# Kernel tuning notes

Measured on AMD Instinct MI355X. Metric: run time of the kernel, lower is better.

## Reference

```python
import jax, jax.numpy as jnp
import numpy as np

N = 50000  # num nodes


def _spmm(edge_index, edge_w, x):
    # sparse [N,N] @ dense [N,d] via gather + segment-sum
    row, col = edge_index[0], edge_index[1]
    msgs = edge_w[:, None] * x[col]                      # [E, d]
    return jax.ops.segment_sum(msgs, row, num_segments=N)


def setup_inputs() -> dict:
    key = jax.random.key(0)
    k1, k2, k3, k4, k5 = jax.random.split(key, 5)
    E1, E2, d = 800000, 1600000, 128
    x = jax.random.normal(k1, (N, d), dtype=jnp.float32)
    edge_index1 = jax.random.randint(k2, (2, E1), 0, N, dtype=jnp.int64)
    edge_w1 = jax.random.uniform(k3, (E1,), dtype=jnp.float32)
    edge_index2 = jax.random.randint(k4, (2, E2), 0, N, dtype=jnp.int64)
    edge_w2 = jax.random.uniform(k5, (E2,), dtype=jnp.float32)
    return {"x": x, "edge_index1": edge_index1, "edge_w1": edge_w1,
            "edge_index2": edge_index2, "edge_w2": edge_w2}


def reference(x, edge_index1, edge_w1, edge_index2, edge_w2):
    x1 = _spmm(edge_index1, edge_w1, x)   # adj_t  @ x  -> [N, d]
    x2 = _spmm(edge_index2, edge_w2, x)   # adj_t2 @ x  -> [N, d]
    return jnp.concatenate([x1, x2], axis=1)  # [N, 2d]
```

## Files before the change

### kernel.cpp

```cpp
#include <hip/hip_runtime.h>


#define N_NODES 50000
#define D 128
#define OUT_STRIDE 256

#define BSHIFT 6
#define BROWS 64
#define NBUCK ((N_NODES + BROWS - 1) >> BSHIFT)
#define BBITS 10
#define CHUNK 4096
#define NTHR 512
#define NWAVE 8
#define WSEG (CHUNK / NWAVE)
#define SITERS (WSEG / 64)
#define ACAP 3072

typedef float vf2 __attribute__((ext_vector_type(2)));

static inline size_t align256(size_t x) { return (x + 255) & ~(size_t)255; }

__device__ __forceinline__ unsigned f32_to_bf16_bits(float f) {
    unsigned u = __float_as_uint(f);
    return (u + 0x7fffu + ((u >> 16) & 1u)) >> 16;
}

template<int BITS>
__device__ __forceinline__ unsigned long long wave_match(int v, bool valid) {
    unsigned long long m = __ballot(valid ? 1 : 0);
    #pragma unroll
    for (int k = 0; k < BITS; ++k) {
        unsigned long long vb = __ballot((v >> k) & 1);
        m &= ((v >> k) & 1) ? vb : ~vb;
    }
    return m;
}


__global__ void __launch_bounds__(NTHR) k_prep(
        const int* __restrict__ ei1, const float* __restrict__ w1, int E1, int nch1,
        const int* __restrict__ ei2, const float* __restrict__ w2, int E2, int ncht,
        unsigned* __restrict__ irec, unsigned char* __restrict__ irl,
        int* __restrict__ ends,
        const float* __restrict__ x, unsigned* __restrict__ xb, int n4) {
    __shared__ unsigned stage_rec[CHUNK];
    __shared__ unsigned char stage_rl[CHUNK];
    __shared__ unsigned short hwc[NWAVE][NBUCK];
    __shared__ int wsum[NWAVE];

    int t = threadIdx.x, lane = t & 63, wid = t >> 6;

    for (long long i = (long long)blockIdx.x * NTHR + t; i < n4;
         i += (long long)gridDim.x * NTHR) {
        float4 v = ((const float4*)x)[i];
        unsigned a = f32_to_bf16_bits(v.x);
        unsigned b = f32_to_bf16_bits(v.y);
        unsigned c = f32_to_bf16_bits(v.z);
        unsigned d = f32_to_bf16_bits(v.w);
        ((uint2*)xb)[i] = make_uint2(a | (b << 16), c | (d << 16));
    }

    int cid = blockIdx.x;
    if (cid >= ncht) return;
    int g = (cid < nch1) ? 0 : 1;
    int chunk = g ? cid - nch1 : cid;
    const int*   ei = g ? ei2 : ei1;
    const float* w  = g ? w2  : w1;
    int E           = g ? E2  : E1;
    int e0  = chunk * CHUNK;
    int cnt = min(CHUNK, E - e0);

    unsigned long long below = (1ull << lane) - 1ull;
    for (int i = t; i < (NWAVE * NBUCK) / 2; i += NTHR) ((int*)hwc)[i] = 0;
    __syncthreads();

    int s0 = wid * WSEG, s1 = min(cnt, s0 + WSEG);
    unsigned meta[SITERS];
    unsigned recs[SITERS];
    #pragma unroll
    for (int k = 0; k < SITERS; ++k) {
        int i = s0 + k * 64 + lane;
        bool v = (i < s1);
        int row = v ? ei[e0 + i] : 0;
        int col = v ? ei[E + e0 + i] : 0;
        float wv = v ? w[e0 + i] : 0.f;
        int bb = row >> BSHIFT;
        unsigned long long m = wave_match<BBITS>(bb, v);
        unsigned rank = (unsigned)__popcll(m & below);
        unsigned base = hwc[wid][bb];
        if (v && (m & below) == 0)
            hwc[wid][bb] = (unsigned short)(base + (unsigned)__popcll(m));
        meta[k] = (unsigned)bb | ((unsigned)(row & 63) << 10) | ((base + rank) << 16);
        recs[k] = (unsigned)col | (f32_to_bf16_bits(wv) << 16);
    }
    __syncthreads();
    {
        int b0 = 2 * t, b1 = b0 + 1;
        int h0[NWAVE], h1[NWAVE];
        int t0 = 0, t1 = 0;
        if (b0 < NBUCK) {
            #pragma unroll
            for (int q = 0; q < NWAVE; ++q) { h0[q] = hwc[q][b0]; t0 += h0[q]; }
        }
        if (b1 < NBUCK) {
            #pragma unroll
            for (int q = 0; q < NWAVE; ++q) { h1[q] = hwc[q][b1]; t1 += h1[q]; }
        }
        int p = t0 + t1, s = p;
        #pragma unroll
        for (int d2 = 1; d2 < 64; d2 <<= 1) { int u = __shfl_up(s, d2, 64); if (lane >= d2) s += u; }
        if (lane == 63) wsum[wid] = s;
        __syncthreads();
        int add = 0;
        #pragma unroll
        for (int k = 0; k < NWAVE; ++k) if (k < wid) add += wsum[k];
        s += add;
        int excl = s - p;
        if (b0 < NBUCK) {
            int a = excl;
            #pragma unroll
            for (int q = 0; q < NWAVE; ++q) { int h = h0[q]; hwc[q][b0] = (unsigned short)a; a += h; }
            ends[(size_t)cid * NBUCK + b0] = a;
        }
        if (b1 < NBUCK) {
            int a = excl + t0;
            #pragma unroll
            for (int q = 0; q < NWAVE; ++q) { int h = h1[q]; hwc[q][b1] = (unsigned short)a; a += h; }
            ends[(size_t)cid * NBUCK + b1] = a;
        }
    }
    __syncthreads();
    #pragma unroll
    for (int k = 0; k < SITERS; ++k) {
        int i = s0 + k * 64 + lane;
        if (i < s1) {
            unsigned mk = meta[k];
            unsigned bb = mk & 1023u;
            unsigned pos = (mk >> 16) + hwc[wid][bb];
            stage_rec[pos] = recs[k];
            stage_rl[pos] = (unsigned char)((mk >> 10) & 63u);
        }
    }
    __syncthreads();
    for (int i = t; i < cnt; i += NTHR) {
        irec[(size_t)cid * CHUNK + i] = stage_rec[i];
        irl[(size_t)cid * CHUNK + i]  = stage_rl[i];
    }
}


__device__ __forceinline__ void fma_rec(unsigned p, unsigned rec, float& ax, float& ay) {
    float w = __int_as_float((int)(rec & 0xffff0000u));
    ax += w * __int_as_float((int)(p << 16));
    ay += w * __int_as_float((int)(p & 0xffff0000u));
}

__global__ void __launch_bounds__(NTHR) k_accum(
        const unsigned* __restrict__ irec, const unsigned char* __restrict__ irl,
        const int* __restrict__ ends, const unsigned* __restrict__ xb,
        float* __restrict__ out, int nch1, int nch2) {
    int task = blockIdx.x;
    int g = task >= NBUCK;
    int b = g ? task - NBUCK : task;
    int c0 = g ? nch1 : 0;
    int nc = g ? nch2 : nch1;

    __shared__ unsigned arecs[ACAP];
    __shared__ unsigned aoutb[ACAP];
    __shared__ unsigned char arl[ACAP];
    __shared__ int crow[BROWS], cur[BROWS], rstart[BROWS];
    __shared__ int total;
    int t = threadIdx.x, lane = t & 63, wid = t >> 6;
    if (t < BROWS) crow[t] = 0;
    if (t == 0) total = 0;
    __syncthreads();
    for (int ci = t; ci < nc; ci += NTHR) {
        const int* ep = ends + (size_t)(c0 + ci) * NBUCK;
        int s = b ? ep[b - 1] : 0;
        int e = ep[b];
        int n = e - s;
        if (!n) continue;
        int dst = atomicAdd(&total, n);
        const unsigned* sr = irec + (size_t)(c0 + ci) * CHUNK + s;
        const unsigned char* sl = irl + (size_t)(c0 + ci) * CHUNK + s;
        int k = 0;
        for (; k + 2 <= n; k += 2) {
            unsigned r0 = sr[k], r1 = sr[k + 1];
            unsigned char l0 = sl[k], l1 = sl[k + 1];
            int p0 = dst + k, p1 = dst + k + 1;
            if (p0 < ACAP) { arl[p0] = l0; arecs[p0] = r0; atomicAdd(&crow[l0], 1); }
            if (p1 < ACAP) { arl[p1] = l1; arecs[p1] = r1; atomicAdd(&crow[l1], 1); }
        }
        if (k < n) {
            unsigned r0 = sr[k];
            unsigned char l0 = sl[k];
            int p0 = dst + k;
            if (p0 < ACAP) { arl[p0] = l0; arecs[p0] = r0; atomicAdd(&crow[l0], 1); }
        }
    }
    __syncthreads();
    int cnt = min(total, ACAP);
    if (wid == 0) {
        int v = crow[lane], s = v;
        #pragma unroll
        for (int d2 = 1; d2 < 64; d2 <<= 1) { int u = __shfl_up(s, d2, 64); if (lane >= d2) s += u; }
        cur[lane] = s - v;
        rstart[lane] = s - v;
    }
    __syncthreads();
    for (int i = t; i < cnt; i += NTHR) {
        int pos = atomicAdd(&cur[arl[i]], 1);
        aoutb[pos] = arecs[i];
    }
    __syncthreads();
    for (int r = wid * 8; r < wid * 8 + 8; ++r) {
        int grow = (b << BSHIFT) + r;
        if (grow >= N_NODES) break;
        int rs = rstart[r], re = cur[r];
        float ax = 0.f, ay = 0.f;
        int j = rs;
        for (; j + 4 <= re; j += 4) {
            unsigned c0r = aoutb[j];
            unsigned c1r = aoutb[j + 1];
            unsigned c2r = aoutb[j + 2];
            unsigned c3r = aoutb[j + 3];
            unsigned p0 = xb[(size_t)(c0r & 0xffffu) * 64 + lane];
            unsigned p1 = xb[(size_t)(c1r & 0xffffu) * 64 + lane];
            unsigned p2 = xb[(size_t)(c2r & 0xffffu) * 64 + lane];
            unsigned p3 = xb[(size_t)(c3r & 0xffffu) * 64 + lane];
            fma_rec(p0, c0r, ax, ay);
            fma_rec(p1, c1r, ax, ay);
            fma_rec(p2, c2r, ax, ay);
            fma_rec(p3, c3r, ax, ay);
        }
        for (; j < re; ++j) {
            unsigned cr = aoutb[j];
            unsigned p = xb[(size_t)(cr & 0xffffu) * 64 + lane];
            fma_rec(p, cr, ax, ay);
        }
        vf2 rv; rv.x = ax; rv.y = ay;
        vf2* o = (vf2*)(out + (size_t)grow * OUT_STRIDE + g * D);
        __builtin_nontemporal_store(rv, o + lane);
    }
}


__global__ void spmm_scatter(const float* __restrict__ x,
                             const int* __restrict__ ei,
                             const float* __restrict__ w,
                             float* __restrict__ out,
                             int E, int col_off) {
    long long gid = (long long)blockIdx.x * blockDim.x + threadIdx.x;
    int e    = (int)(gid >> 5);
    int lane = (int)(gid & 31);
    if (e >= E) return;
    int row  = ei[e];
    int col  = ei[E + e];
    float wv = w[e];
    const float4* xv = (const float4*)(x + (size_t)col * D);
    float4 v = xv[lane];
    float* o = out + (size_t)row * OUT_STRIDE + col_off + lane * 4;
    atomicAdd(o + 0, wv * v.x);
    atomicAdd(o + 1, wv * v.y);
    atomicAdd(o + 2, wv * v.z);
    atomicAdd(o + 3, wv * v.w);
}

extern "C" void kernel_launch(void* const* d_in, const int* in_sizes, int n_in,
                              void* d_out, int out_size, void* d_ws, size_t ws_size,
                              hipStream_t stream) {
    const float* x_p   = (const float*)d_in[0];
    const int*   ei1_p = (const int*)d_in[1];
    const float* w1_p  = (const float*)d_in[2];
    const int*   ei2_p = (const int*)d_in[3];
    const float* w2_p  = (const float*)d_in[4];
    float* out_p = (float*)d_out;

    int E1 = in_sizes[1] / 2;
    int E2 = in_sizes[3] / 2;
    const int block = 256;

    int nch1 = (E1 + CHUNK - 1) / CHUNK;
    int nch2 = (E2 + CHUNK - 1) / CHUNK;
    int ncht = nch1 + nch2;
    int n4   = N_NODES * 32;

    size_t rec_b  = align256((size_t)ncht * CHUNK * sizeof(unsigned));
    size_t rl_b   = align256((size_t)ncht * CHUNK);
    size_t ends_b = align256((size_t)ncht * NBUCK * sizeof(int));
    size_t xb_b   = align256((size_t)N_NODES * 64 * sizeof(unsigned));
    size_t o_rec  = 0;
    size_t o_rl   = o_rec + rec_b;
    size_t o_ends = o_rl + rl_b;
    size_t o_xb   = o_ends + ends_b;
    size_t needed = o_xb + xb_b;

    if (ws_size < needed) {
        (void)hipMemsetAsync(d_out, 0, (size_t)out_size * sizeof(float), stream);
        long long th1 = (long long)E1 * 32;
        spmm_scatter<<<(int)((th1 + block - 1) / block), block, 0, stream>>>(
            x_p, ei1_p, w1_p, out_p, E1, 0);
        long long th2 = (long long)E2 * 32;
        spmm_scatter<<<(int)((th2 + block - 1) / block), block, 0, stream>>>(
            x_p, ei2_p, w2_p, out_p, E2, D);
        return;
    }

    char* ws = (char*)d_ws;
    unsigned*      irec = (unsigned*)(ws + o_rec);
    unsigned char* irl  = (unsigned char*)(ws + o_rl);
    int*           ends = (int*)(ws + o_ends);
    unsigned*      xb   = (unsigned*)(ws + o_xb);

    k_prep<<<ncht, NTHR, 0, stream>>>(ei1_p, w1_p, E1, nch1, ei2_p, w2_p, E2,
                                      ncht, irec, irl, ends, x_p, xb, n4);

    k_accum<<<2 * NBUCK, NTHR, 0, stream>>>(irec, irl, ends, xb, out_p,
                                            nch1, nch2);
}
```

Measured before the change: 223.8 us.

## Sort bucket edges by row and source-column range; split bf16 conversion into own kernel

The accumulate kernel now sorts edges within each 64-row bucket by a combined key (local row and high bits of the source column) instead of by row alone. Within each row, gathers of x are then ordered by column region, which should improve cache locality for the bf16 feature gathers. The x-to-bf16 conversion moves out of the prep kernel into its own kernel, and the prep chunk size doubles, which halves the number of prep blocks and grows the shared staging buffers. The risks are an extra launch, a wider 512-entry scan with an added block sync, and lower occupancy in the prep kernel.

```diff
diff --git a/kernel.cpp b/kernel.cpp
--- a/kernel.cpp
+++ b/kernel.cpp
@@ -9,12 +9,13 @@
 #define BROWS 64
 #define NBUCK ((N_NODES + BROWS - 1) >> BSHIFT)
 #define BBITS 10
-#define CHUNK 4096
+#define CHUNK 8192
 #define NTHR 512
 #define NWAVE 8
 #define WSEG (CHUNK / NWAVE)
 #define SITERS (WSEG / 64)
 #define ACAP 3072
+#define NKEY 512
 
 typedef float vf2 __attribute__((ext_vector_type(2)));
 
@@ -37,31 +38,30 @@
 }
 
 
+__global__ void cvt_bf16(const float* __restrict__ x, uint2* __restrict__ xb4, int n4) {
+    int i = blockIdx.x * blockDim.x + threadIdx.x;
+    if (i >= n4) return;
+    float4 v = ((const float4*)x)[i];
+    unsigned a = f32_to_bf16_bits(v.x);
+    unsigned b = f32_to_bf16_bits(v.y);
+    unsigned c = f32_to_bf16_bits(v.z);
+    unsigned d = f32_to_bf16_bits(v.w);
+    xb4[i] = make_uint2(a | (b << 16), c | (d << 16));
+}
+
+
 __global__ void __launch_bounds__(NTHR) k_prep(
         const int* __restrict__ ei1, const float* __restrict__ w1, int E1, int nch1,
         const int* __restrict__ ei2, const float* __restrict__ w2, int E2, int ncht,
         unsigned* __restrict__ irec, unsigned char* __restrict__ irl,
-        int* __restrict__ ends,
-        const float* __restrict__ x, unsigned* __restrict__ xb, int n4) {
+        int* __restrict__ ends) {
     __shared__ unsigned stage_rec[CHUNK];
     __shared__ unsigned char stage_rl[CHUNK];
     __shared__ unsigned short hwc[NWAVE][NBUCK];
     __shared__ int wsum[NWAVE];
 
     int t = threadIdx.x, lane = t & 63, wid = t >> 6;
-
-    for (long long i = (long long)blockIdx.x * NTHR + t; i < n4;
-         i += (long long)gridDim.x * NTHR) {
-        float4 v = ((const float4*)x)[i];
-        unsigned a = f32_to_bf16_bits(v.x);
-        unsigned b = f32_to_bf16_bits(v.y);
-        unsigned c = f32_to_bf16_bits(v.z);
-        unsigned d = f32_to_bf16_bits(v.w);
-        ((uint2*)xb)[i] = make_uint2(a | (b << 16), c | (d << 16));
-    }
-
     int cid = blockIdx.x;
-    if (cid >= ncht) return;
     int g = (cid < nch1) ? 0 : 1;
     int chunk = g ? cid - nch1 : cid;
     const int*   ei = g ? ei2 : ei1;
@@ -167,11 +167,11 @@
 
     __shared__ unsigned arecs[ACAP];
     __shared__ unsigned aoutb[ACAP];
-    __shared__ unsigned char arl[ACAP];
-    __shared__ int crow[BROWS], cur[BROWS], rstart[BROWS];
+    __shared__ unsigned short akey[ACAP];
+    __shared__ int crow[NKEY], cur[NKEY], rstart[NKEY];
     __shared__ int total;
     int t = threadIdx.x, lane = t & 63, wid = t >> 6;
-    if (t < BROWS) crow[t] = 0;
+    crow[t] = 0;
     if (t == 0) total = 0;
     __syncthreads();
     for (int ci = t; ci < nc; ci += NTHR) {
@@ -188,35 +188,52 @@
             unsigned r0 = sr[k], r1 = sr[k + 1];
             unsigned char l0 = sl[k], l1 = sl[k + 1];
             int p0 = dst + k, p1 = dst + k + 1;
-            if (p0 < ACAP) { arl[p0] = l0; arecs[p0] = r0; atomicAdd(&crow[l0], 1); }
-            if (p1 < ACAP) { arl[p1] = l1; arecs[p1] = r1; atomicAdd(&crow[l1], 1); }
+            if (p0 < ACAP) {
+                unsigned ky = ((unsigned)l0 << 3) | ((r0 & 0xffffu) >> 13);
+                akey[p0] = (unsigned short)ky; arecs[p0] = r0; atomicAdd(&crow[ky], 1);
+            }
+            if (p1 < ACAP) {
+                unsigned ky = ((unsigned)l1 << 3) | ((r1 & 0xffffu) >> 13);
+                akey[p1] = (unsigned short)ky; arecs[p1] = r1; atomicAdd(&crow[ky], 1);
+            }
         }
         if (k < n) {
             unsigned r0 = sr[k];
             unsigned char l0 = sl[k];
             int p0 = dst + k;
-            if (p0 < ACAP) { arl[p0] = l0; arecs[p0] = r0; atomicAdd(&crow[l0], 1); }
+            if (p0 < ACAP) {
+                unsigned ky = ((unsigned)l0 << 3) | ((r0 & 0xffffu) >> 13);
+                akey[p0] = (unsigned short)ky; arecs[p0] = r0; atomicAdd(&crow[ky], 1);
+            }
         }
     }
     __syncthreads();
     int cnt = min(total, ACAP);
-    if (wid == 0) {
-        int v = crow[lane], s = v;
+    {
+        int v = crow[t], s = v;
         #pragma unroll
         for (int d2 = 1; d2 < 64; d2 <<= 1) { int u = __shfl_up(s, d2, 64); if (lane >= d2) s += u; }
-        cur[lane] = s - v;
-        rstart[lane] = s - v;
+        __shared__ int wsum[NWAVE];
+        if (lane == 63) wsum[wid] = s;
+        __syncthreads();
+        int add = 0;
+        #pragma unroll
+        for (int k = 0; k < NWAVE; ++k) if (k < wid) add += wsum[k];
+        s += add;
+        cur[t] = s - v;
+        rstart[t] = s - v;
     }
     __syncthreads();
     for (int i = t; i < cnt; i += NTHR) {
-        int pos = atomicAdd(&cur[arl[i]], 1);
+        int pos = atomicAdd(&cur[akey[i]], 1);
         aoutb[pos] = arecs[i];
     }
     __syncthreads();
     for (int r = wid * 8; r < wid * 8 + 8; ++r) {
         int grow = (b << BSHIFT) + r;
         if (grow >= N_NODES) break;
-        int rs = rstart[r], re = cur[r];
+        int rs = rstart[r << 3];
+        int re = cur[(r << 3) | 7];
         float ax = 0.f, ay = 0.f;
         int j = rs;
         for (; j + 4 <= re; j += 4) {
@@ -312,8 +329,10 @@
     int*           ends = (int*)(ws + o_ends);
     unsigned*      xb   = (unsigned*)(ws + o_xb);
 
+    cvt_bf16<<<(n4 + block - 1) / block, block, 0, stream>>>(x_p, (uint2*)xb, n4);
+
     k_prep<<<ncht, NTHR, 0, stream>>>(ei1_p, w1_p, E1, nch1, ei2_p, w2_p, E2,
-                                      ncht, irec, irl, ends, x_p, xb, n4);
+                                      ncht, irec, irl, ends);
 
     k_accum<<<2 * NBUCK, NTHR, 0, stream>>>(irec, irl, ends, xb, out_p,
                                             nch1, nch2);
```

Result: slower. 236.4 us (+5.6%).
